# Optimization experiments

Hardware: AMD Instinct MI355X
Metric: run time of the kernel (lower is better)

## Reference

```python
import jax, jax.numpy as jnp
import numpy as np

C = 128
B, H, W = 32, 64, 64


def _lstm(x, Wih, Whh, b, reverse):
    """Batched LSTM, PyTorch gate order (i, f, g, o).
    x: [N, T, C] -> h: [N, T, C]. reverse=True scans backward but returns
    outputs aligned to the original time axis (matches torch bidirectional)."""
    N = x.shape[0]
    Ch = Whh.shape[1]
    xp = jnp.einsum('ntc,gc->ntg', x, Wih) + b  # precomputed input projection [N,T,4C]

    def step(carry, xt):
        h, c = carry
        z = xt + h @ Whh.T
        i, f, g, o = jnp.split(z, 4, axis=-1)
        c = jax.nn.sigmoid(f) * c + jax.nn.sigmoid(i) * jnp.tanh(g)
        h = jax.nn.sigmoid(o) * jnp.tanh(c)
        return (h, c), h

    init = (jnp.zeros((N, Ch), x.dtype), jnp.zeros((N, Ch), x.dtype))
    _, hs = jax.lax.scan(step, init, jnp.swapaxes(xp, 0, 1), reverse=reverse)
    return jnp.swapaxes(hs, 0, 1)


def _conv1x1(x, w, b):
    # x: [B, C, s1, s2]; w: [O, C]; b: [O]
    return jnp.einsum('bcxy,oc->boxy', x, w) + b[None, :, None, None]


def setup_inputs() -> dict:
    key = jax.random.key(0)
    ks = jax.random.split(key, 24)
    k = 1.0 / np.sqrt(C)
    u = lambda kk, shp: jax.random.uniform(kk, shp, jnp.float32, -k, k)
    inp = {'x': jax.random.normal(ks[0], (B, C, H, W), jnp.float32)}
    names = ['vWih_f', 'vWhh_f', 'vb_f', 'vWih_b', 'vWhh_b', 'vb_b',
             'hWih_f', 'hWhh_f', 'hb_f', 'hWih_b', 'hWhh_b', 'hb_b']
    shapes = [(4 * C, C), (4 * C, C), (4 * C,)] * 4
    for i, (n, s) in enumerate(zip(names, shapes)):
        inp[n] = u(ks[1 + i], s)
    for i, n in enumerate(['down', 'up', 'right', 'left']):
        inp['w_' + n] = u(ks[13 + 2 * i], (C, C))
        inp['b_' + n] = u(ks[14 + 2 * i], (C,))
    return inp


def reference(x, vWih_f, vWhh_f, vb_f, vWih_b, vWhh_b, vb_b,
              hWih_f, hWhh_f, hb_f, hWih_b, hWhh_b, hb_b,
              w_down, b_down, w_up, b_up, w_right, b_right, w_left, b_left):
    Bn, Cn, Hn, Wn = x.shape
    xt = jnp.transpose(x, (0, 3, 2, 1))  # [B, W, H, C]  (torch transpose(1,3))

    # vertical LSTM: torch loops i over H, seq over W -> batch rows into B*H
    xv = jnp.transpose(xt, (0, 2, 1, 3)).reshape(Bn * Hn, Wn, Cn)  # [B*H, W, C]
    hv_f = _lstm(xv, vWih_f, vWhh_f, vb_f, False).reshape(Bn, Hn, Wn, Cn)
    hv_b = _lstm(xv, vWih_b, vWhh_b, vb_b, True).reshape(Bn, Hn, Wn, Cn)
    # stack over H at dim2 then transpose(1,3) -> [B, C, H, W]
    x_up = _conv1x1(jnp.transpose(hv_f, (0, 3, 1, 2)), w_up, b_up)
    x_down = _conv1x1(jnp.transpose(hv_b, (0, 3, 1, 2)), w_down, b_down)

    # horizontal LSTM: torch loops i over W, seq over H -> batch cols into B*W
    xh = xt.reshape(Bn * Wn, Hn, Cn)  # [B*W, H, C]
    hh_f = _lstm(xh, hWih_f, hWhh_f, hb_f, False).reshape(Bn, Wn, Hn, Cn)
    hh_b = _lstm(xh, hWih_b, hWhh_b, hb_b, True).reshape(Bn, Wn, Hn, Cn)
    # stack over W at dim2 gives [B, H, W, C]; transpose(1,3) -> [B, C, W, H]
    x_right = _conv1x1(jnp.transpose(hh_f, (0, 3, 1, 2)), w_right, b_right)
    x_left = _conv1x1(jnp.transpose(hh_b, (0, 3, 1, 2)), w_left, b_left)

    return (x_down, x_up, x_right, x_left)
```

## Files before the change

### kernel.cpp

```cpp
#include <hip/hip_runtime.h>
#include <stdint.h>

#define OUTSZ  (32*128*64*64)

typedef short bf16x8 __attribute__((ext_vector_type(8)));
typedef float f32x4  __attribute__((ext_vector_type(4)));

__device__ __forceinline__ uint16_t f2bf(float f) {
  union { float f; uint32_t u; } v; v.f = f;
  uint32_t u = v.u;
  u += 0x7fffu + ((u >> 16) & 1u);
  return (uint16_t)(u >> 16);
}

__device__ __forceinline__ float sigf(float x) {
  return __builtin_amdgcn_rcpf(1.f + __expf(-x));
}
__device__ __forceinline__ float tanh_(float x) {
  float ax = fabsf(x);
  float e  = __expf(-2.f * ax);
  float t  = (1.f - e) * __builtin_amdgcn_rcpf(1.f + e);
  return copysignf(t, x);
}

__global__ void transpose_x(const float* __restrict__ x, uint16_t* __restrict__ xn) {
  const int h = blockIdx.x, b = blockIdx.y;
  __shared__ float tile[128][65];
  const int tid = threadIdx.x;
  #pragma unroll
  for (int it = 0; it < 32; ++it) {
    int idx = it * 256 + tid;
    int c = idx >> 6, w = idx & 63;
    tile[c][w] = x[(((b * 128 + c) * 64 + h) << 6) + w];
  }
  __syncthreads();
  uint32_t* out = (uint32_t*)(xn + ((size_t)(b * 64 + h) * 64) * 128);
  #pragma unroll
  for (int it = 0; it < 16; ++it) {
    int idx = it * 256 + tid;
    int w = idx >> 6, cd = idx & 63;
    uint32_t lo = f2bf(tile[cd * 2][w]);
    uint32_t hi = f2bf(tile[cd * 2 + 1][w]);
    out[w * 64 + cd] = lo | (hi << 16);
  }
}

struct PrepArgs { const float* s[12]; };

__global__ void prep_weights(PrepArgs a, uint16_t* __restrict__ wbuf,
                             uint16_t* __restrict__ wcbuf) {
  int idx = blockIdx.x * 256 + threadIdx.x;
  if (idx < 524288) {
    int m = idx >> 16;
    wbuf[idx] = f2bf(a.s[m][idx & 65535]);
  } else {
    int j = idx - 524288;
    if (j < 65536) {
      int m = j >> 14;
      wcbuf[j] = f2bf(a.s[8 + m][j & 16383]);
    }
  }
}

__global__ __launch_bounds__(512, 2) void lstm_kernel(
    const uint16_t* __restrict__ xn,
    const uint16_t* __restrict__ wbuf,
    const float* __restrict__ bvf, const float* __restrict__ bvb,
    const float* __restrict__ bhf, const float* __restrict__ bhb,
    uint16_t* __restrict__ hbuf)
{
  const int dir  = blockIdx.y;
  const int seq0 = blockIdx.x * 32;
  const int tid  = threadIdx.x;
  const int wv   = tid >> 6;
  const int lane = tid & 63;
  const int l15  = lane & 15;
  const int l4   = lane >> 4;
  const int mycol = wv * 16 + l15;
  const bool rev   = (dir & 1);
  const bool horiz = (dir >= 2);

  const uint16_t* wih = wbuf + (size_t)(2 * dir) * (512 * 128);
  const uint16_t* whh = wih + 512 * 128;
  const float* bias = (dir == 0) ? bvf : (dir == 1) ? bvb : (dir == 2) ? bhf : bhb;
  uint16_t* hout = hbuf + (size_t)dir * ((size_t)2048 * 64 * 128);

  bf16x8 Bih[4][4], Bhh[4][4];
  {
    const int base = mycol * 128 + l4 * 8;
    #pragma unroll
    for (int g = 0; g < 4; ++g)
      #pragma unroll
      for (int kc = 0; kc < 4; ++kc) {
        Bih[g][kc] = *(const bf16x8*)(wih + base + g * (128 * 128) + kc * 32);
        Bhh[g][kc] = *(const bf16x8*)(whh + base + g * (128 * 128) + kc * 32);
      }
  }
  float bia[4];
  #pragma unroll
  for (int g = 0; g < 4; ++g) bia[g] = bias[mycol + 128 * g];

  __shared__ __attribute__((aligned(16))) uint16_t ring[8][32][136];
  {
    uint32_t* p = (uint32_t*)&ring[7][0][0];
    for (int i = tid; i < 2176; i += 512) p[i] = 0;
  }
  __syncthreads();

  int xbase[2];
  #pragma unroll
  for (int mt = 0; mt < 2; ++mt) {
    int seq = seq0 + mt * 16 + l15;
    xbase[mt] = horiz ? (((seq >> 6) * 4096 + (seq & 63)) * 128)
                      : (seq * (64 * 128));
  }
  const int tstride = horiz ? (64 * 128) : 128;

  float cst[2][4];
  #pragma unroll
  for (int mt = 0; mt < 2; ++mt)
    #pragma unroll
    for (int r = 0; r < 4; ++r) cst[mt][r] = 0.f;

  const int drow   = tid >> 4;
  const int dchunk = tid & 15;
  const int dpc8   = dchunk ^ ((drow >> 2) & 3);

  auto dump_slot = [&](int g, int s) {
    bf16x8 v = *(const bf16x8*)(&ring[s][drow][dpc8 * 8]);
    int stepl = g * 8 + s;
    int t = rev ? 63 - stepl : stepl;
    *(bf16x8*)(hout + ((size_t)(seq0 + drow) * 64 + t) * 128 + dchunk * 8) = v;
  };

  const int swz = (l15 >> 2) & 3;
  const f32x4 vzero = {0.f, 0.f, 0.f, 0.f};

  auto do_step = [&](int step, bf16x8 (&axc)[2][4], bf16x8 (&axn)[2][4]) {
    const int tn_l = (step < 63) ? step + 1 : 63;
    const int tn   = rev ? 63 - tn_l : tn_l;
    #pragma unroll
    for (int mt = 0; mt < 2; ++mt)
      #pragma unroll
      for (int kc = 0; kc < 4; ++kc)
        axn[mt][kc] = *(const bf16x8*)(xn + xbase[mt] + tn * tstride + kc * 32 + l4 * 8);

    if (step >= 7) dump_slot(((step + 1) >> 3) - 1, (step + 1) & 7);

    const int prev = (step + 7) & 7;
    f32x4 acc[2][4];
    #pragma unroll
    for (int mt = 0; mt < 2; ++mt)
      #pragma unroll
      for (int g = 0; g < 4; ++g) acc[mt][g] = vzero;

    #pragma unroll
    for (int kc = 0; kc < 4; ++kc) {
      bf16x8 ah[2];
      #pragma unroll
      for (int mt = 0; mt < 2; ++mt)
        ah[mt] = *(const bf16x8*)(&ring[prev][mt * 16 + l15][((kc * 4 + l4) ^ swz) * 8]);
      #pragma unroll
      for (int mt = 0; mt < 2; ++mt)
        #pragma unroll
        for (int g = 0; g < 4; ++g) {
          acc[mt][g] = __builtin_amdgcn_mfma_f32_16x16x32_bf16(axc[mt][kc], Bih[g][kc], acc[mt][g], 0, 0, 0);
          acc[mt][g] = __builtin_amdgcn_mfma_f32_16x16x32_bf16(ah[mt],      Bhh[g][kc], acc[mt][g], 0, 0, 0);
        }
    }

    const int slot = step & 7;
    #pragma unroll
    for (int mt = 0; mt < 2; ++mt)
      #pragma unroll
      for (int r = 0; r < 4; ++r) {
        float zi = acc[mt][0][r] + bia[0];
        float zf = acc[mt][1][r] + bia[1];
        float zg = acc[mt][2][r] + bia[2];
        float zo = acc[mt][3][r] + bia[3];
        float c = sigf(zf) * cst[mt][r] + sigf(zi) * tanh_(zg);
        cst[mt][r] = c;
        float h = sigf(zo) * tanh_(c);
        int row = mt * 16 + l4 * 4 + r;
        ring[slot][row][((mycol >> 3) ^ l4) * 8 + (mycol & 7)] = f2bf(h);
      }
    __syncthreads();
  };

  bf16x8 axA[2][4], axB[2][4];
  {
    const int t0 = rev ? 63 : 0;
    #pragma unroll
    for (int mt = 0; mt < 2; ++mt)
      #pragma unroll
      for (int kc = 0; kc < 4; ++kc)
        axA[mt][kc] = *(const bf16x8*)(xn + xbase[mt] + t0 * tstride + kc * 32 + l4 * 8);
  }
  for (int s2 = 0; s2 < 64; s2 += 2) {
    do_step(s2,     axA, axB);
    do_step(s2 + 1, axB, axA);
  }
  #pragma unroll
  for (int s = 1; s < 8; ++s) dump_slot(7, s);
}

__global__ __launch_bounds__(256, 2) void conv_kernel(
    const uint16_t* __restrict__ hbuf, const uint16_t* __restrict__ wc,
    const float* __restrict__ b_down, const float* __restrict__ b_up,
    const float* __restrict__ b_right, const float* __restrict__ b_left,
    float* __restrict__ out)
{
  const int d   = blockIdx.y;
  const int P0  = blockIdx.x * 128;
  const int tid = threadIdx.x;
  const int wv = tid >> 6, lane = tid & 63, l15 = lane & 15, l4 = lane >> 4;

  const int lstm_dir = (d == 0) ? 1 : (d == 1) ? 0 : d;
  const uint16_t* hb = hbuf + (size_t)lstm_dir * ((size_t)2048 * 64 * 128);
  const uint16_t* w  = wc + d * (128 * 128);
  const float* bias = (d == 0) ? b_down : (d == 1) ? b_up : (d == 2) ? b_right : b_left;
  float* outp = out + (size_t)d * OUTSZ;

  bf16x8 Bf[2][4];
  float bc[2];
  #pragma unroll
  for (int j = 0; j < 2; ++j) {
    int o = (2 * wv + j) * 16 + l15;
    bc[j] = bias[o];
    #pragma unroll
    for (int kc = 0; kc < 4; ++kc)
      Bf[j][kc] = *(const bf16x8*)(w + o * 128 + kc * 32 + l4 * 8);
  }

  const f32x4 vzero = {0.f, 0.f, 0.f, 0.f};
  f32x4 acc[8][2];
  #pragma unroll
  for (int mt = 0; mt < 8; ++mt) { acc[mt][0] = vzero; acc[mt][1] = vzero; }

  #pragma unroll
  for (int kc = 0; kc < 4; ++kc) {
    bf16x8 A[8];
    #pragma unroll
    for (int mt = 0; mt < 8; ++mt) {
      int p = P0 + mt * 16 + l15;
      A[mt] = *(const bf16x8*)(hb + (size_t)p * 128 + kc * 32 + l4 * 8);
    }
    #pragma unroll
    for (int mt = 0; mt < 8; ++mt)
      #pragma unroll
      for (int j = 0; j < 2; ++j)
        acc[mt][j] = __builtin_amdgcn_mfma_f32_16x16x32_bf16(A[mt], Bf[j][kc], acc[mt][j], 0, 0, 0);
  }

  __shared__ __attribute__((aligned(16))) float olds[64][132];
  const int bb = P0 >> 12, s0 = P0 & 4095;
  float* obase = outp + ((size_t)bb * 128) * 4096 + s0;

  #pragma unroll
  for (int j = 0; j < 2; ++j) {
    if (j) __syncthreads();
    #pragma unroll
    for (int mt = 0; mt < 8; ++mt) {
      f32x4 v = acc[mt][j] + bc[j];
      *(f32x4*)(&olds[wv * 16 + l15][(mt * 4 + l4) * 4]) = v;
    }
    __syncthreads();
    #pragma unroll
    for (int it = 0; it < 8; ++it) {
      int flat = (it * 256 + tid) * 4;
      int ol = flat >> 7, s = flat & 127;
      int o = (ol >> 4) * 32 + j * 16 + (ol & 15);
      f32x4 v = *(const f32x4*)(&olds[ol][s]);
      *(f32x4*)(obase + (size_t)o * 4096 + s) = v;
    }
  }
}

extern "C" void kernel_launch(void* const* d_in, const int* in_sizes, int n_in,
                              void* d_out, int out_size, void* d_ws, size_t ws_size,
                              hipStream_t stream) {
  const float* x = (const float*)d_in[0];
  uint16_t* ws    = (uint16_t*)d_ws;
  uint16_t* xn    = ws;
  uint16_t* wbuf  = xn + 16777216;
  uint16_t* wcbuf = wbuf + 524288;
  uint16_t* hbuf  = wcbuf + 65536;

  transpose_x<<<dim3(64, 32), 256, 0, stream>>>(x, xn);

  PrepArgs pa;
  const int widx[12] = {1, 2, 4, 5, 7, 8, 10, 11, 13, 15, 17, 19};
  for (int i = 0; i < 12; ++i) pa.s[i] = (const float*)d_in[widx[i]];
  prep_weights<<<2304, 256, 0, stream>>>(pa, wbuf, wcbuf);

  lstm_kernel<<<dim3(64, 4), 512, 0, stream>>>(
      xn, wbuf,
      (const float*)d_in[3], (const float*)d_in[6],
      (const float*)d_in[9], (const float*)d_in[12],
      hbuf);

  conv_kernel<<<dim3(1024, 4), 256, 0, stream>>>(
      hbuf, wcbuf,
      (const float*)d_in[14], (const float*)d_in[16],
      (const float*)d_in[18], (const float*)d_in[20],
      (float*)d_out);
}
```

Before: 598.9 us.

## Hoist input-projection MFMAs for the next step before the barrier, off the critical path

The input-to-hidden MFMAs for step t+1 now run right after the gate nonlinearities of step t, before the barrier. They seed the accumulators with the bias, so only the hidden-to-hidden MFMAs stay on the serial recurrence chain. The bias adds in the gate math are dropped, and tanh switches to a cheaper 2*sigmoid(2x)-1 form without the abs and copysign. __syncthreads becomes an explicit lgkmcnt wait, s_barrier and sched_barrier. The accumulators stay live across steps, which adds register pressure, and the new tanh may overflow or lose accuracy for large negative inputs.

```diff
diff --git a/kernel.cpp b/kernel.cpp
--- a/kernel.cpp
+++ b/kernel.cpp
@@ -16,11 +16,9 @@
 __device__ __forceinline__ float sigf(float x) {
   return __builtin_amdgcn_rcpf(1.f + __expf(-x));
 }
-__device__ __forceinline__ float tanh_(float x) {
-  float ax = fabsf(x);
-  float e  = __expf(-2.f * ax);
-  float t  = (1.f - e) * __builtin_amdgcn_rcpf(1.f + e);
-  return copysignf(t, x);
+__device__ __forceinline__ float tanh2s(float x) {
+  float e = __expf(-2.f * x);
+  return __builtin_amdgcn_rcpf(1.f + e) * 2.f - 1.f;
 }
 
 __global__ void transpose_x(const float* __restrict__ x, uint16_t* __restrict__ xn) {
@@ -134,9 +132,28 @@
   };
 
   const int swz = (l15 >> 2) & 3;
-  const f32x4 vzero = {0.f, 0.f, 0.f, 0.f};
+
+  f32x4 acc[2][4];
+
+  auto ih_accum = [&](bf16x8 (&ax)[2][4]) {
+    #pragma unroll
+    for (int mt = 0; mt < 2; ++mt)
+      #pragma unroll
+      for (int g = 0; g < 4; ++g) {
+        f32x4 bs = {bia[g], bia[g], bia[g], bia[g]};
+        acc[mt][g] = bs;
+      }
+    #pragma unroll
+    for (int kc = 0; kc < 4; ++kc)
+      #pragma unroll
+      for (int mt = 0; mt < 2; ++mt)
+        #pragma unroll
+        for (int g = 0; g < 4; ++g)
+          acc[mt][g] = __builtin_amdgcn_mfma_f32_16x16x32_bf16(ax[mt][kc], Bih[g][kc], acc[mt][g], 0, 0, 0);
+  };
 
   auto do_step = [&](int step, bf16x8 (&axc)[2][4], bf16x8 (&axn)[2][4]) {
+    (void)axc;
     const int tn_l = (step < 63) ? step + 1 : 63;
     const int tn   = rev ? 63 - tn_l : tn_l;
     #pragma unroll
@@ -148,12 +165,6 @@
     if (step >= 7) dump_slot(((step + 1) >> 3) - 1, (step + 1) & 7);
 
     const int prev = (step + 7) & 7;
-    f32x4 acc[2][4];
-    #pragma unroll
-    for (int mt = 0; mt < 2; ++mt)
-      #pragma unroll
-      for (int g = 0; g < 4; ++g) acc[mt][g] = vzero;
-
     #pragma unroll
     for (int kc = 0; kc < 4; ++kc) {
       bf16x8 ah[2];
@@ -163,10 +174,8 @@
       #pragma unroll
       for (int mt = 0; mt < 2; ++mt)
         #pragma unroll
-        for (int g = 0; g < 4; ++g) {
-          acc[mt][g] = __builtin_amdgcn_mfma_f32_16x16x32_bf16(axc[mt][kc], Bih[g][kc], acc[mt][g], 0, 0, 0);
-          acc[mt][g] = __builtin_amdgcn_mfma_f32_16x16x32_bf16(ah[mt],      Bhh[g][kc], acc[mt][g], 0, 0, 0);
-        }
+        for (int g = 0; g < 4; ++g)
+          acc[mt][g] = __builtin_amdgcn_mfma_f32_16x16x32_bf16(ah[mt], Bhh[g][kc], acc[mt][g], 0, 0, 0);
     }
 
     const int slot = step & 7;
@@ -174,17 +183,22 @@
     for (int mt = 0; mt < 2; ++mt)
       #pragma unroll
       for (int r = 0; r < 4; ++r) {
-        float zi = acc[mt][0][r] + bia[0];
-        float zf = acc[mt][1][r] + bia[1];
-        float zg = acc[mt][2][r] + bia[2];
-        float zo = acc[mt][3][r] + bia[3];
-        float c = sigf(zf) * cst[mt][r] + sigf(zi) * tanh_(zg);
+        float zi = acc[mt][0][r];
+        float zf = acc[mt][1][r];
+        float zg = acc[mt][2][r];
+        float zo = acc[mt][3][r];
+        float c = sigf(zf) * cst[mt][r] + sigf(zi) * tanh2s(zg);
         cst[mt][r] = c;
-        float h = sigf(zo) * tanh_(c);
+        float h = sigf(zo) * tanh2s(c);
         int row = mt * 16 + l4 * 4 + r;
         ring[slot][row][((mycol >> 3) ^ l4) * 8 + (mycol & 7)] = f2bf(h);
       }
-    __syncthreads();
+
+    if (step < 63) ih_accum(axn);
+
+    asm volatile("s_waitcnt lgkmcnt(0)" ::: "memory");
+    __builtin_amdgcn_s_barrier();
+    __builtin_amdgcn_sched_barrier(0);
   };
 
   bf16x8 axA[2][4], axB[2][4];
@@ -196,6 +210,7 @@
       for (int kc = 0; kc < 4; ++kc)
         axA[mt][kc] = *(const bf16x8*)(xn + xbase[mt] + t0 * tstride + kc * 32 + l4 * 8);
   }
+  ih_accum(axA);
   for (int s2 = 0; s2 < 64; s2 += 2) {
     do_step(s2,     axA, axB);
     do_step(s2 + 1, axB, axA);
```

Result: no change. 587.6 us (-1.9%).
